# Performance work log

Hardware: AMD Instinct MI355X
Metric: run time of the kernel (lower is better)

Reference implementation:

```python
import jax, jax.numpy as jnp
import numpy as np

N_NODES = 100000
N_EDGES = 1600000
IN_DIM = 128
HID = 64
OUT_DIM = 3


def _glorot(key, shape):
    fan_in, fan_out = shape[0], shape[1]
    std = (2.0 / (fan_in + fan_out)) ** 0.5
    return jax.random.normal(key, shape, jnp.float32) * std


def setup_inputs() -> dict:
    key = jax.random.key(0)
    ks = jax.random.split(key, 12)
    x = jax.random.normal(ks[0], (N_NODES, IN_DIM), jnp.float32)
    edge_index = jax.random.randint(ks[1], (2, N_EDGES), 0, N_NODES, dtype=jnp.int32)
    return {
        "x": x,
        "edge_index": edge_index,
        "W1": _glorot(ks[2], (IN_DIM, HID)), "b1": jnp.zeros((HID,), jnp.float32),
        "W2": _glorot(ks[3], (HID, HID)), "b2": jnp.zeros((HID,), jnp.float32),
        "W3": _glorot(ks[4], (HID, HID)), "b3": jnp.zeros((HID,), jnp.float32),
        "W4": _glorot(ks[5], (HID, HID // 2)), "b4": jnp.zeros((HID // 2,), jnp.float32),
        "Wh": _glorot(ks[6], (HID // 2, OUT_DIM)), "bh": jnp.zeros((OUT_DIM,), jnp.float32),
    }


def reference(x, edge_index, W1, b1, W2, b2, W3, b3, W4, b4, Wh, bh):
    n = x.shape[0]
    self_loops = jnp.arange(n, dtype=edge_index.dtype)
    src = jnp.concatenate([edge_index[0], self_loops])  # message sources j
    dst = jnp.concatenate([edge_index[1], self_loops])  # aggregation targets i
    # symmetric GCN normalization with self-loops: deg over targets (unit edge weights)
    deg = jax.ops.segment_sum(jnp.ones_like(dst, jnp.float32), dst, num_segments=n)
    dinv = jnp.where(deg > 0, jax.lax.rsqrt(deg), 0.0)
    norm = dinv[src] * dinv[dst]  # [E+N]

    def gcn(h, W, b):
        h = h @ W  # transform first (PyG GCNConv order)
        agg = jax.ops.segment_sum(h[src] * norm[:, None], dst, num_segments=n)
        return agg + b

    h = jax.nn.relu(gcn(x, W1, b1))   # dropout is identity in eval mode
    h = jax.nn.relu(gcn(h, W2, b2))
    h = jax.nn.relu(gcn(h, W3, b3))
    h = jax.nn.relu(gcn(h, W4, b4))
    return h @ Wh + bh  # [N, 3]
```

## Files before the change

kernel.cpp:

```cpp
#include <hip/hip_runtime.h>
#include <hip/hip_bf16.h>
#include <hip/hip_fp16.h>
#include <cstdint>


#define MAXD 512
#define EB   8192
#define PADSLACK 2048

typedef _Float16 half8v __attribute__((ext_vector_type(8)));
typedef _Float16 half2v __attribute__((ext_vector_type(2)));
typedef float    float4v __attribute__((ext_vector_type(4)));

#if defined(__has_builtin)
#if __has_builtin(__builtin_amdgcn_fdot2)
#define HAVE_FDOT2 1
#endif
#endif

__device__ __forceinline__ float fdot2f(half2v a, half2v b, float c) {
#ifdef HAVE_FDOT2
    return __builtin_amdgcn_fdot2(a, b, c, false);
#else
    return c + (float)a[0] * (float)b[0] + (float)a[1] * (float)b[1];
#endif
}

__device__ __forceinline__ void digit_base_scan(const int* __restrict__ totals,
                                                int ND, int* pairs, int* cbs) {
    const int t = threadIdx.x;
    const int e0 = 2 * t, e1 = 2 * t + 1;
    int v0 = (e0 < ND) ? totals[e0] : 0;
    int v1 = (e1 < ND) ? totals[e1] : 0;
    pairs[t] = v0 + v1;
    __syncthreads();
    for (int off = 1; off < 256; off <<= 1) {
        int x = (t >= off) ? pairs[t - off] : 0;
        __syncthreads();
        pairs[t] += x;
        __syncthreads();
    }
    int ep = pairs[t] - v0 - v1;
    cbs[e0] = ep;
    cbs[e1] = ep + v0;
    __syncthreads();
}

__device__ __forceinline__ void hist_body(const int* __restrict__ ei,
                                          int* __restrict__ histM, int E, int b) {
    __shared__ int hist[MAXD];
    const int tid = threadIdx.x;
    hist[tid] = 0; hist[tid + 256] = 0;
    __syncthreads();
    const int base = b * EB;
#pragma unroll 2
    for (int it = 0; it < EB / 256; it += 4) {
        int d[4]; bool ok[4];
#pragma unroll
        for (int u = 0; u < 4; ++u) {
            int e = base + (it + u) * 256 + tid;
            ok[u] = e < E;
            d[u] = ok[u] ? ei[E + e] : 0;
        }
#pragma unroll
        for (int u = 0; u < 4; ++u)
            if (ok[u]) atomicAdd(&hist[d[u] >> 8], 1);
    }
    __syncthreads();
    histM[(size_t)b * MAXD + tid] = hist[tid];
    histM[(size_t)b * MAXD + tid + 256] = hist[tid + 256];
}

__global__ __launch_bounds__(256) void scan_digits_k(int* __restrict__ histM,
                                                     int* __restrict__ totals,
                                                     int NBLK) {
    __shared__ int s[256];
    const int t = threadIdx.x, dg = blockIdx.x;
    int v = (t < NBLK) ? histM[(size_t)t * MAXD + dg] : 0;
    s[t] = v;
    __syncthreads();
    for (int off = 1; off < 256; off <<= 1) {
        int x = (t >= off) ? s[t - off] : 0;
        __syncthreads();
        s[t] += x;
        __syncthreads();
    }
    if (t < NBLK) histM[(size_t)t * MAXD + dg] = s[t] - v;
    if (t == 255) totals[dg] = s[255];
}

template <int K, int OUT>
__device__ __forceinline__ void gemm_body(const float* __restrict__ H,
                                          const float* __restrict__ W,
                                          float* __restrict__ Tout, int n, int bx) {
    constexpr int TX  = OUT / 4;
    constexpr int TY  = 256 / TX;
    constexpr int BM  = TY * 4;
    constexpr int BK  = 32;
    constexpr int PAD = 4;

    __shared__ float At[BK][BM + PAD];
    __shared__ float Ws[BK][OUT];

    const int t    = threadIdx.x;
    const int cx   = t % TX;
    const int ry   = t / TX;
    const int row0 = bx * BM;

    float acc[4][4] = {{0.f}};
    const int arow = t >> 3;
    const int af4  = t & 7;

    for (int k0 = 0; k0 < K; k0 += BK) {
#pragma unroll
        for (int p = 0; p < BM / 32; ++p) {
            int r  = arow + p * 32;
            int gr = row0 + r;
            int grc = gr < n ? gr : n - 1;
            float4 v = *reinterpret_cast<const float4*>(
                H + (size_t)grc * K + k0 + af4 * 4);
            At[af4 * 4 + 0][r] = v.x;
            At[af4 * 4 + 1][r] = v.y;
            At[af4 * 4 + 2][r] = v.z;
            At[af4 * 4 + 3][r] = v.w;
        }
#pragma unroll
        for (int p = 0; p < (BK * OUT) / 1024; ++p) {
            int idx = t + p * 256;
            int wk  = idx / (OUT / 4);
            int wf  = idx % (OUT / 4);
            float4 v = *reinterpret_cast<const float4*>(
                W + (size_t)(k0 + wk) * OUT + wf * 4);
            *reinterpret_cast<float4*>(&Ws[wk][wf * 4]) = v;
        }
        __syncthreads();
#pragma unroll
        for (int k = 0; k < BK; ++k) {
            float4 a = *reinterpret_cast<const float4*>(&At[k][ry * 4]);
            float4 w = *reinterpret_cast<const float4*>(&Ws[k][cx * 4]);
            acc[0][0] = fmaf(a.x, w.x, acc[0][0]);
            acc[0][1] = fmaf(a.x, w.y, acc[0][1]);
            acc[0][2] = fmaf(a.x, w.z, acc[0][2]);
            acc[0][3] = fmaf(a.x, w.w, acc[0][3]);
            acc[1][0] = fmaf(a.y, w.x, acc[1][0]);
            acc[1][1] = fmaf(a.y, w.y, acc[1][1]);
            acc[1][2] = fmaf(a.y, w.z, acc[1][2]);
            acc[1][3] = fmaf(a.y, w.w, acc[1][3]);
            acc[2][0] = fmaf(a.z, w.x, acc[2][0]);
            acc[2][1] = fmaf(a.z, w.y, acc[2][1]);
            acc[2][2] = fmaf(a.z, w.z, acc[2][2]);
            acc[2][3] = fmaf(a.z, w.w, acc[2][3]);
            acc[3][0] = fmaf(a.w, w.x, acc[3][0]);
            acc[3][1] = fmaf(a.w, w.y, acc[3][1]);
            acc[3][2] = fmaf(a.w, w.z, acc[3][2]);
            acc[3][3] = fmaf(a.w, w.w, acc[3][3]);
        }
        __syncthreads();
    }
#pragma unroll
    for (int i = 0; i < 4; ++i) {
        int gr = row0 + ry * 4 + i;
        if (gr < n) {
            float4 v = make_float4(acc[i][0], acc[i][1], acc[i][2], acc[i][3]);
            *reinterpret_cast<float4*>(Tout + (size_t)gr * OUT + cx * 4) = v;
        }
    }
}

__device__ __forceinline__ void pack_body(const int* __restrict__ ei,
                                          const int* __restrict__ histM,
                                          const int* __restrict__ totals,
                                          int* __restrict__ packed,
                                          int E, int ND, int b) {
    __shared__ int pairs[256];
    __shared__ int cbs[MAXD];
    __shared__ int cur[MAXD];
    const int tid = threadIdx.x;
    digit_base_scan(totals, ND, pairs, cbs);
    for (int t = tid; t < ND; t += 256)
        cur[t] = cbs[t] + histM[(size_t)b * MAXD + t];
    __syncthreads();
    const int base = b * EB;
    for (int it = 0; it < EB / 256; it += 4) {
        int s[4], d[4]; bool ok[4];
#pragma unroll
        for (int u = 0; u < 4; ++u) {
            int e = base + (it + u) * 256 + tid;
            ok[u] = e < E;
            if (ok[u]) { s[u] = ei[e]; d[u] = ei[E + e]; }
        }
#pragma unroll
        for (int u = 0; u < 4; ++u) {
            if (ok[u]) {
                int pos = atomicAdd(&cur[d[u] >> 8], 1);
                packed[pos] = (s[u] << 8) | (d[u] & 255);
            }
        }
    }
}

__global__ __launch_bounds__(256) void hist_gemm1_k(
    const int* __restrict__ ei, int* __restrict__ histM, int E,
    const float* __restrict__ x, const float* __restrict__ W1,
    float* __restrict__ T1, int n, int NH) {
    const int bx = blockIdx.x;
    if (bx < NH) hist_body(ei, histM, E, bx);
    else         gemm_body<128, 64>(x, W1, T1, n, bx - NH);
}

__global__ __launch_bounds__(256) void pack_gemm1_k(
    const int* __restrict__ ei, const int* __restrict__ histM,
    const int* __restrict__ totals, int* __restrict__ packed,
    const float* __restrict__ x, const float* __restrict__ W1,
    float* __restrict__ T1, int n, int E, int ND, int NPB, int G1) {
    const int bx = blockIdx.x;
    if (bx < NPB) pack_body(ei, histM, totals, packed, E, ND, bx);
    else          gemm_body<128, 64>(x, W1, T1, n, G1 + bx - NPB);
}

__global__ __launch_bounds__(256) void bucket_k(const int* __restrict__ packed,
                                                const int* __restrict__ totals,
                                                int ND,
                                                int* __restrict__ col,
                                                int4* __restrict__ rpc,
                                                float* __restrict__ dinv,
                                                const float* __restrict__ Traw,
                                                __half* __restrict__ Th, int n) {
    __shared__ int   pairs[256];
    __shared__ int   cbs[MAXD];
    __shared__ int   hist[256];
    __shared__ int   pref[256];
    __shared__ int   cur[256];
    __shared__ float dinv_l[256];

    const int tid = threadIdx.x;
    const int dg  = blockIdx.x;
    digit_base_scan(totals, ND, pairs, cbs);
    const int base  = cbs[dg];
    const int m     = totals[dg];
    const int basep = base + dg * PADSLACK;

    hist[tid] = 0;
    __syncthreads();
    for (int k0 = 0; k0 < m; k0 += 1024) {
        int v[4]; bool ok[4];
#pragma unroll
        for (int u = 0; u < 4; ++u) {
            int k = k0 + u * 256 + tid;
            ok[u] = k < m;
            v[u] = ok[u] ? packed[base + k] : 0;
        }
#pragma unroll
        for (int u = 0; u < 4; ++u)
            if (ok[u]) atomicAdd(&hist[v[u] & 255], 1);
    }
    __syncthreads();
    const int deg   = hist[tid];
    const int cnt_p = (deg + 8) & ~7;
    pref[tid] = cnt_p;
    __syncthreads();
    for (int off = 1; off < 256; off <<= 1) {
        int x = (tid >= off) ? pref[tid - off] : 0;
        __syncthreads();
        pref[tid] += x;
        __syncthreads();
    }
    const int rp = basep + pref[tid] - cnt_p;
    const float di = rsqrtf((float)(deg + 1));
    dinv_l[tid] = di;
    cur[tid] = rp + 1;
    const int d = dg * 256 + tid;
    if (d < n) {
        rpc[d]  = make_int4(rp, cnt_p, __float_as_int(di), 0);
        dinv[d] = di;
        col[rp] = d;
        for (int k = deg + 1; k < cnt_p; ++k) col[rp + k] = n;
    }
    __syncthreads();
    for (int k0 = 0; k0 < m; k0 += 1024) {
        int v[4]; bool ok[4];
#pragma unroll
        for (int u = 0; u < 4; ++u) {
            int k = k0 + u * 256 + tid;
            ok[u] = k < m;
            v[u] = ok[u] ? packed[base + k] : 0;
        }
#pragma unroll
        for (int u = 0; u < 4; ++u) {
            if (ok[u]) {
                int pos = atomicAdd(&cur[v[u] & 255], 1);
                col[pos] = v[u] >> 8;
            }
        }
    }
    const int r0 = dg * 256;
#pragma unroll 4
    for (int it = 0; it < 16; ++it) {
        int idx = it * 256 + tid;
        int rl  = idx >> 4;
        int r   = r0 + rl;
        if (r < n) {
            float4 v = reinterpret_cast<const float4*>(Traw)[(size_t)r * 16 + (idx & 15)];
            float dd = dinv_l[rl];
            union { ushort4 u; __half h[4]; } pk;
            pk.h[0] = __float2half_rn(v.x * dd);
            pk.h[1] = __float2half_rn(v.y * dd);
            pk.h[2] = __float2half_rn(v.z * dd);
            pk.h[3] = __float2half_rn(v.w * dd);
            reinterpret_cast<ushort4*>(Th)[(size_t)r * 16 + (idx & 15)] = pk.u;
        }
    }
    if (dg == 0 && tid < 16) {
        uint2 z; z.x = 0u; z.y = 0u;
        reinterpret_cast<uint2*>(Th)[(size_t)n * 16 + tid] = z;
    }
}

template <int OUT>
__global__ __launch_bounds__(256) void gemm_mfma_k(
    const _Float16* __restrict__ H, const float* __restrict__ W,
    const float* __restrict__ dinv, _Float16* __restrict__ T, int n) {
    constexpr int NT = OUT / 16;
    const int lane = threadIdx.x & 63;
    const int m16  = lane & 15;
    const int quad = lane >> 4;
    const int wid  = (blockIdx.x * blockDim.x + threadIdx.x) >> 6;
    const int nw   = (gridDim.x * blockDim.x) >> 6;

    half8v bfrag[NT][2];
#pragma unroll
    for (int t = 0; t < NT; ++t)
#pragma unroll
        for (int h = 0; h < 2; ++h)
#pragma unroll
            for (int j = 0; j < 8; ++j)
                bfrag[t][h][j] = (_Float16)W[(size_t)(h * 32 + quad * 8 + j) * OUT
                                             + t * 16 + m16];

    const int nblk = (n + 15) >> 4;
    for (int rb = wid; rb < nblk; rb += nw) {
        const int r0 = rb * 16;
        int ra = r0 + m16; if (ra >= n) ra = n - 1;
        const half8v* hrow = reinterpret_cast<const half8v*>(H + (size_t)ra * 64);
        half8v a0 = hrow[quad];
        half8v a1 = hrow[4 + quad];

        float4v dfr[NT];
#pragma unroll
        for (int t = 0; t < NT; ++t) {
            float4v z = {0.f, 0.f, 0.f, 0.f};
            z = __builtin_amdgcn_mfma_f32_16x16x32_f16(a0, bfrag[t][0], z, 0, 0, 0);
            z = __builtin_amdgcn_mfma_f32_16x16x32_f16(a1, bfrag[t][1], z, 0, 0, 0);
            dfr[t] = z;
        }
#pragma unroll
        for (int reg = 0; reg < 4; ++reg) {
            int row = r0 + quad * 4 + reg;
            if (row < n) {
                float di = dinv[row];
#pragma unroll
                for (int t = 0; t < NT; ++t)
                    T[(size_t)row * 64 + t * 16 + m16] =
                        (_Float16)(dfr[t][reg] * di);
            }
        }
    }
}

template <int NB, int LR>
__device__ __forceinline__ void gather_batch(int c_l, const uint2* __restrict__ T2,
                                             int q, int sw, float4& acc, int g0) {
    constexpr int NSW = 64 / LR;
    constexpr int GPE = 8 / NSW;
    constexpr int NV  = NB * GPE;
    const half2v s10 = {(_Float16)1.f, (_Float16)0.f};
    const half2v s01 = {(_Float16)0.f, (_Float16)1.f};
    uint2 v[NV];
#pragma unroll
    for (int g = 0; g < NB; ++g)
#pragma unroll
        for (int u = 0; u < GPE; ++u) {
            int cc = __shfl(c_l, (g0 + g) * 8 + u * NSW + sw, 64);
            v[g * GPE + u] = T2[(size_t)cc * 16 + q];
        }
#pragma unroll
    for (int k = 0; k < NV; ++k) {
        union { uint2 uu; half2v h[2]; } cv; cv.uu = v[k];
        acc.x = fdot2f(cv.h[0], s10, acc.x);
        acc.y = fdot2f(cv.h[0], s01, acc.y);
        acc.z = fdot2f(cv.h[1], s10, acc.z);
        acc.w = fdot2f(cv.h[1], s01, acc.w);
    }
}

__device__ __forceinline__ void gather_node(int cnt, int start, int c_a,
                                            const uint2* __restrict__ T2,
                                            const int* __restrict__ col,
                                            int lane, int q, int sw, float4& acc) {
    if (cnt <= 64) {
        switch (cnt >> 3) {
            case 1: gather_batch<1, 64 / ((64/16))>(c_a, T2, q, sw, acc, 0); break;
            default: break;
        }
    }
}

template <int LR, bool FUSE_HEAD>
__global__ __launch_bounds__(256, 8) void agg_k(const __half* __restrict__ T,
                                             const int4* __restrict__ rpc,
                                             const int* __restrict__ col,
                                             const float* __restrict__ bias,
                                             void* __restrict__ O, int n,
                                             const float* __restrict__ Wh,
                                             const float* __restrict__ bh) {
    constexpr int NSW = 64 / LR;
    constexpr int GPE = 8 / NSW;
    const int lane = threadIdx.x & 63;
    const int q    = lane % LR;
    const int sw   = lane / LR;
    const int wid  = (blockIdx.x * blockDim.x + threadIdx.x) >> 6;
    const int nw   = (gridDim.x * blockDim.x) >> 6;
    if (wid >= n) return;

    const uint2* __restrict__ T2 = reinterpret_cast<const uint2*>(T);
    const float4 b4 = reinterpret_cast<const float4*>(bias)[q];

    int ib = wid + nw; if (ib >= n) ib = n - 1;
    int4 rc_a = rpc[wid];
    int4 rc_b = rpc[ib];
    int  c_a  = col[rc_a.x + lane];

    for (int i = wid; i < n; i += nw) {
        int ic = i + 2 * nw; if (ic >= n) ic = n - 1;
        int4 rc_c = rpc[ic];
        int  c_nx = col[rc_b.x + lane];

        const int   cnt   = rc_a.y;
        const int   start = rc_a.x;
        const float di    = __int_as_float(rc_a.z);

        float4 acc = make_float4(0.f, 0.f, 0.f, 0.f);
        if (cnt <= 64) {
            switch (cnt >> 3) {
                case 1: gather_batch<1, LR>(c_a, T2, q, sw, acc, 0); break;
                case 2: gather_batch<2, LR>(c_a, T2, q, sw, acc, 0); break;
                case 3: gather_batch<3, LR>(c_a, T2, q, sw, acc, 0); break;
                case 4: gather_batch<4, LR>(c_a, T2, q, sw, acc, 0); break;
                case 5: gather_batch<4, LR>(c_a, T2, q, sw, acc, 0);
                        gather_batch<1, LR>(c_a, T2, q, sw, acc, 4); break;
                case 6: gather_batch<4, LR>(c_a, T2, q, sw, acc, 0);
                        gather_batch<2, LR>(c_a, T2, q, sw, acc, 4); break;
                case 7: gather_batch<4, LR>(c_a, T2, q, sw, acc, 0);
                        gather_batch<3, LR>(c_a, T2, q, sw, acc, 4); break;
                default: gather_batch<4, LR>(c_a, T2, q, sw, acc, 0);
                         gather_batch<4, LR>(c_a, T2, q, sw, acc, 4); break;
            }
        } else {
            for (int base = 0; base < cnt; base += 64) {
                int m = cnt - base; if (m > 64) m = 64;
                int c_l = col[start + base + lane];
                for (int jg = 0; jg < m; jg += 32) {
                    int nb2 = (m - jg) >> 3; if (nb2 > 4) nb2 = 4;
                    int g0 = jg >> 3;
                    switch (nb2) {
                        case 1: gather_batch<1, LR>(c_l, T2, q, sw, acc, g0); break;
                        case 2: gather_batch<2, LR>(c_l, T2, q, sw, acc, g0); break;
                        case 3: gather_batch<3, LR>(c_l, T2, q, sw, acc, g0); break;
                        default: gather_batch<4, LR>(c_l, T2, q, sw, acc, g0); break;
                    }
                }
            }
        }
#pragma unroll
        for (int off = LR; off < 64; off <<= 1) {
            acc.x += __shfl_xor(acc.x, off, 64);
            acc.y += __shfl_xor(acc.y, off, 64);
            acc.z += __shfl_xor(acc.z, off, 64);
            acc.w += __shfl_xor(acc.w, off, 64);
        }
        float4 h;
        h.x = fmaxf(fmaf(di, acc.x, b4.x), 0.f);
        h.y = fmaxf(fmaf(di, acc.y, b4.y), 0.f);
        h.z = fmaxf(fmaf(di, acc.z, b4.z), 0.f);
        h.w = fmaxf(fmaf(di, acc.w, b4.w), 0.f);
        if constexpr (!FUSE_HEAD) {
            if (sw == 0) {
                union { ushort4 u; __half hh[4]; } pk;
                pk.hh[0] = __float2half_rn(h.x);
                pk.hh[1] = __float2half_rn(h.y);
                pk.hh[2] = __float2half_rn(h.z);
                pk.hh[3] = __float2half_rn(h.w);
                ushort* base_p = (ushort*)O + (size_t)i * 64;
                *reinterpret_cast<ushort4*>(base_p + 4 * q) = pk.u;
            }
        } else {
            float* Of = (float*)O;
            float p0 = h.x * Wh[(4 * q + 0) * 3 + 0];
            float p1 = h.x * Wh[(4 * q + 0) * 3 + 1];
            float p2 = h.x * Wh[(4 * q + 0) * 3 + 2];
            p0 = fmaf(h.y, Wh[(4 * q + 1) * 3 + 0], p0);
            p1 = fmaf(h.y, Wh[(4 * q + 1) * 3 + 1], p1);
            p2 = fmaf(h.y, Wh[(4 * q + 1) * 3 + 2], p2);
            p0 = fmaf(h.z, Wh[(4 * q + 2) * 3 + 0], p0);
            p1 = fmaf(h.z, Wh[(4 * q + 2) * 3 + 1], p1);
            p2 = fmaf(h.z, Wh[(4 * q + 2) * 3 + 2], p2);
            p0 = fmaf(h.w, Wh[(4 * q + 3) * 3 + 0], p0);
            p1 = fmaf(h.w, Wh[(4 * q + 3) * 3 + 1], p1);
            p2 = fmaf(h.w, Wh[(4 * q + 3) * 3 + 2], p2);
#pragma unroll
            for (int off = 1; off < LR; off <<= 1) {
                p0 += __shfl_xor(p0, off, 64);
                p1 += __shfl_xor(p1, off, 64);
                p2 += __shfl_xor(p2, off, 64);
            }
            if (lane == 0) {
                Of[(size_t)i * 3 + 0] = p0 + bh[0];
                Of[(size_t)i * 3 + 1] = p1 + bh[1];
                Of[(size_t)i * 3 + 2] = p2 + bh[2];
            }
        }
        rc_a = rc_b; rc_b = rc_c; c_a = c_nx;
    }
}

extern "C" void kernel_launch(void* const* d_in, const int* in_sizes, int n_in,
                              void* d_out, int out_size, void* d_ws, size_t ws_size,
                              hipStream_t stream) {
    const float* x  = (const float*)d_in[0];
    const int*   ei = (const int*)d_in[1];
    const float* W1 = (const float*)d_in[2];
    const float* b1 = (const float*)d_in[3];
    const float* W2 = (const float*)d_in[4];
    const float* b2 = (const float*)d_in[5];
    const float* W3 = (const float*)d_in[6];
    const float* b3 = (const float*)d_in[7];
    const float* W4 = (const float*)d_in[8];
    const float* b4 = (const float*)d_in[9];
    const float* Wh = (const float*)d_in[10];
    const float* bh = (const float*)d_in[11];
    float* out = (float*)d_out;

    const int n = in_sizes[0] / 128;
    const int E = in_sizes[1] / 2;
    const int ND   = (n + 255) / 256;
    const int NBLK = (E + EB - 1) / EB;

    char* ws = (char*)d_ws;
    auto alloc = [&](size_t bytes) {
        char* p = ws;
        ws += (bytes + 255) & ~(size_t)255;
        return p;
    };
    int*    histM  = (int*)alloc((size_t)NBLK * MAXD * 4);
    int*    totals = (int*)alloc((size_t)MAXD * 4);
    int*    packed = (int*)alloc((size_t)E * 4);
    int*    col    = (int*)alloc(((size_t)E + (size_t)ND * PADSLACK + 256) * 4);
    int4*   rpc    = (int4*)alloc((size_t)n * 16);
    float*  dinv   = (float*)alloc((size_t)n * 4);
    float*  bufF   = (float*)alloc((size_t)n * 64 * 4);
    __half* bufH   = (__half*)alloc(((size_t)n + 1) * 64 * 2);
    __half* bufG   = (__half*)bufF;

    dim3 blk(256);
    const int G  = (n + 63) / 64;
    const int G1 = G / 3;
    const int G2 = G - G1;
    const int agg_blocks = 2048;
    const int mfma_blocks = 640;

    hist_gemm1_k<<<dim3(NBLK + G1), blk, 0, stream>>>(ei, histM, E, x, W1, bufF, n, NBLK);
    scan_digits_k<<<dim3(ND), blk, 0, stream>>>(histM, totals, NBLK);
    pack_gemm1_k<<<dim3(NBLK + G2), blk, 0, stream>>>(ei, histM, totals, packed,
                                                      x, W1, bufF, n, E, ND, NBLK, G1);
    bucket_k<<<dim3(ND), blk, 0, stream>>>(packed, totals, ND, col, rpc,
                                           dinv, bufF, bufH, n);
    agg_k<16, false><<<dim3(agg_blocks), blk, 0, stream>>>(
        bufH, rpc, col, b1, bufG, n, nullptr, nullptr);
    gemm_mfma_k<64><<<dim3(mfma_blocks), blk, 0, stream>>>(
        (const _Float16*)bufG, W2, dinv, (_Float16*)bufH, n);
    agg_k<16, false><<<dim3(agg_blocks), blk, 0, stream>>>(
        bufH, rpc, col, b2, bufG, n, nullptr, nullptr);
    gemm_mfma_k<64><<<dim3(mfma_blocks), blk, 0, stream>>>(
        (const _Float16*)bufG, W3, dinv, (_Float16*)bufH, n);
    agg_k<16, false><<<dim3(agg_blocks), blk, 0, stream>>>(
        bufH, rpc, col, b3, bufG, n, nullptr, nullptr);
    gemm_mfma_k<32><<<dim3(mfma_blocks), blk, 0, stream>>>(
        (const _Float16*)bufG, W4, dinv, (_Float16*)bufH, n);
    agg_k<8, true><<<dim3(agg_blocks), blk, 0, stream>>>(
        bufH, rpc, col, b4, out, n, Wh, bh);
}
```

Before: 334.5 us.

## Software-pipeline neighbor gathers across nodes with double-buffered registers

Restructures the aggregation kernel so the first four groups of neighbor feature loads for the next node are issued before the current node's accumulation, using two register buffers that swap roles in an unrolled-by-two loop. Row-pointer and column prefetch depth is extended by one node. Launch bounds drop from 8 to 4 waves per SIMD to allow the larger register footprint. This aims to hide gather latency but reduces occupancy and raises register pressure.

```diff
diff --git a/kernel.cpp b/kernel.cpp
--- a/kernel.cpp
+++ b/kernel.cpp
@@ -368,6 +368,37 @@
 }
 
 template <int NB, int LR>
+__device__ __forceinline__ void gather_issue(int c_l, const uint2* __restrict__ T2,
+                                             int q, int sw, uint2* __restrict__ v) {
+    constexpr int NSW = 64 / LR;
+    constexpr int GPE = 8 / NSW;
+#pragma unroll
+    for (int g = 0; g < NB; ++g)
+#pragma unroll
+        for (int u = 0; u < GPE; ++u) {
+            int cc = __shfl(c_l, g * 8 + u * NSW + sw, 64);
+            v[g * GPE + u] = T2[(size_t)cc * 16 + q];
+        }
+}
+
+template <int NG, int LR>
+__device__ __forceinline__ void gather_fdot(const uint2* __restrict__ v, float4& acc) {
+    constexpr int NSW = 64 / LR;
+    constexpr int GPE = 8 / NSW;
+    constexpr int NV  = NG * GPE;
+    const half2v s10 = {(_Float16)1.f, (_Float16)0.f};
+    const half2v s01 = {(_Float16)0.f, (_Float16)1.f};
+#pragma unroll
+    for (int k = 0; k < NV; ++k) {
+        union { uint2 uu; half2v h[2]; } cv; cv.uu = v[k];
+        acc.x = fdot2f(cv.h[0], s10, acc.x);
+        acc.y = fdot2f(cv.h[0], s01, acc.y);
+        acc.z = fdot2f(cv.h[1], s10, acc.z);
+        acc.w = fdot2f(cv.h[1], s01, acc.w);
+    }
+}
+
+template <int NB, int LR>
 __device__ __forceinline__ void gather_batch(int c_l, const uint2* __restrict__ T2,
                                              int q, int sw, float4& acc, int g0) {
     constexpr int NSW = 64 / LR;
@@ -393,70 +424,43 @@
     }
 }
 
-__device__ __forceinline__ void gather_node(int cnt, int start, int c_a,
-                                            const uint2* __restrict__ T2,
-                                            const int* __restrict__ col,
-                                            int lane, int q, int sw, float4& acc) {
-    if (cnt <= 64) {
-        switch (cnt >> 3) {
-            case 1: gather_batch<1, 64 / ((64/16))>(c_a, T2, q, sw, acc, 0); break;
-            default: break;
-        }
-    }
-}
-
 template <int LR, bool FUSE_HEAD>
-__global__ __launch_bounds__(256, 8) void agg_k(const __half* __restrict__ T,
-                                             const int4* __restrict__ rpc,
-                                             const int* __restrict__ col,
-                                             const float* __restrict__ bias,
-                                             void* __restrict__ O, int n,
-                                             const float* __restrict__ Wh,
-                                             const float* __restrict__ bh) {
-    constexpr int NSW = 64 / LR;
-    constexpr int GPE = 8 / NSW;
-    const int lane = threadIdx.x & 63;
-    const int q    = lane % LR;
-    const int sw   = lane / LR;
-    const int wid  = (blockIdx.x * blockDim.x + threadIdx.x) >> 6;
-    const int nw   = (gridDim.x * blockDim.x) >> 6;
-    if (wid >= n) return;
-
-    const uint2* __restrict__ T2 = reinterpret_cast<const uint2*>(T);
-    const float4 b4 = reinterpret_cast<const float4*>(bias)[q];
-
-    int ib = wid + nw; if (ib >= n) ib = n - 1;
-    int4 rc_a = rpc[wid];
-    int4 rc_b = rpc[ib];
-    int  c_a  = col[rc_a.x + lane];
-
-    for (int i = wid; i < n; i += nw) {
-        int ic = i + 2 * nw; if (ic >= n) ic = n - 1;
-        int4 rc_c = rpc[ic];
-        int  c_nx = col[rc_b.x + lane];
-
-        const int   cnt   = rc_a.y;
-        const int   start = rc_a.x;
-        const float di    = __int_as_float(rc_a.z);
-
-        float4 acc = make_float4(0.f, 0.f, 0.f, 0.f);
-        if (cnt <= 64) {
-            switch (cnt >> 3) {
-                case 1: gather_batch<1, LR>(c_a, T2, q, sw, acc, 0); break;
-                case 2: gather_batch<2, LR>(c_a, T2, q, sw, acc, 0); break;
-                case 3: gather_batch<3, LR>(c_a, T2, q, sw, acc, 0); break;
-                case 4: gather_batch<4, LR>(c_a, T2, q, sw, acc, 0); break;
-                case 5: gather_batch<4, LR>(c_a, T2, q, sw, acc, 0);
-                        gather_batch<1, LR>(c_a, T2, q, sw, acc, 4); break;
-                case 6: gather_batch<4, LR>(c_a, T2, q, sw, acc, 0);
-                        gather_batch<2, LR>(c_a, T2, q, sw, acc, 4); break;
-                case 7: gather_batch<4, LR>(c_a, T2, q, sw, acc, 0);
-                        gather_batch<3, LR>(c_a, T2, q, sw, acc, 4); break;
-                default: gather_batch<4, LR>(c_a, T2, q, sw, acc, 0);
-                         gather_batch<4, LR>(c_a, T2, q, sw, acc, 4); break;
-            }
-        } else {
-            for (int base = 0; base < cnt; base += 64) {
+__device__ __forceinline__ void agg_body(
+    int i, int n, int nw, int lane, int q, int sw,
+    const uint2* __restrict__ T2, const int* __restrict__ col,
+    const int4* __restrict__ rpc,
+    int4& rcP, int4& rcQ, int4& rcR, int& cP, int& cQ,
+    uint2* __restrict__ vP, uint2* __restrict__ vQ,
+    const float4& b4, void* __restrict__ O,
+    const float* __restrict__ Wh, const float* __restrict__ bh) {
+    int iS = i + 3 * nw; if (iS >= n) iS = n - 1;
+    int4 rcS = rpc[iS];
+    int cR = col[rcR.x + lane];
+    {
+        int ng = rcQ.y >> 3; if (ng > 4) ng = 4;
+        switch (ng) {
+            case 1: gather_issue<1, LR>(cQ, T2, q, sw, vQ); break;
+            case 2: gather_issue<2, LR>(cQ, T2, q, sw, vQ); break;
+            case 3: gather_issue<3, LR>(cQ, T2, q, sw, vQ); break;
+            default: gather_issue<4, LR>(cQ, T2, q, sw, vQ); break;
+        }
+    }
+    const int   cnt = rcP.y;
+    const float di  = __int_as_float(rcP.z);
+    float4 acc = make_float4(0.f, 0.f, 0.f, 0.f);
+    switch (cnt >> 3) {
+        case 1: gather_fdot<1, LR>(vP, acc); break;
+        case 2: gather_fdot<2, LR>(vP, acc); break;
+        case 3: gather_fdot<3, LR>(vP, acc); break;
+        case 4: gather_fdot<4, LR>(vP, acc); break;
+        case 5: gather_fdot<4, LR>(vP, acc); gather_batch<1, LR>(cP, T2, q, sw, acc, 4); break;
+        case 6: gather_fdot<4, LR>(vP, acc); gather_batch<2, LR>(cP, T2, q, sw, acc, 4); break;
+        case 7: gather_fdot<4, LR>(vP, acc); gather_batch<3, LR>(cP, T2, q, sw, acc, 4); break;
+        default: {
+            gather_fdot<4, LR>(vP, acc);
+            gather_batch<4, LR>(cP, T2, q, sw, acc, 4);
+            const int start = rcP.x;
+            for (int base = 64; base < cnt; base += 64) {
                 int m = cnt - base; if (m > 64) m = 64;
                 int c_l = col[start + base + lane];
                 for (int jg = 0; jg < m; jg += 32) {
@@ -470,56 +474,108 @@
                     }
                 }
             }
-        }
-#pragma unroll
-        for (int off = LR; off < 64; off <<= 1) {
-            acc.x += __shfl_xor(acc.x, off, 64);
-            acc.y += __shfl_xor(acc.y, off, 64);
-            acc.z += __shfl_xor(acc.z, off, 64);
-            acc.w += __shfl_xor(acc.w, off, 64);
-        }
-        float4 h;
-        h.x = fmaxf(fmaf(di, acc.x, b4.x), 0.f);
-        h.y = fmaxf(fmaf(di, acc.y, b4.y), 0.f);
-        h.z = fmaxf(fmaf(di, acc.z, b4.z), 0.f);
-        h.w = fmaxf(fmaf(di, acc.w, b4.w), 0.f);
-        if constexpr (!FUSE_HEAD) {
-            if (sw == 0) {
-                union { ushort4 u; __half hh[4]; } pk;
-                pk.hh[0] = __float2half_rn(h.x);
-                pk.hh[1] = __float2half_rn(h.y);
-                pk.hh[2] = __float2half_rn(h.z);
-                pk.hh[3] = __float2half_rn(h.w);
-                ushort* base_p = (ushort*)O + (size_t)i * 64;
-                *reinterpret_cast<ushort4*>(base_p + 4 * q) = pk.u;
-            }
-        } else {
-            float* Of = (float*)O;
-            float p0 = h.x * Wh[(4 * q + 0) * 3 + 0];
-            float p1 = h.x * Wh[(4 * q + 0) * 3 + 1];
-            float p2 = h.x * Wh[(4 * q + 0) * 3 + 2];
-            p0 = fmaf(h.y, Wh[(4 * q + 1) * 3 + 0], p0);
-            p1 = fmaf(h.y, Wh[(4 * q + 1) * 3 + 1], p1);
-            p2 = fmaf(h.y, Wh[(4 * q + 1) * 3 + 2], p2);
-            p0 = fmaf(h.z, Wh[(4 * q + 2) * 3 + 0], p0);
-            p1 = fmaf(h.z, Wh[(4 * q + 2) * 3 + 1], p1);
-            p2 = fmaf(h.z, Wh[(4 * q + 2) * 3 + 2], p2);
-            p0 = fmaf(h.w, Wh[(4 * q + 3) * 3 + 0], p0);
-            p1 = fmaf(h.w, Wh[(4 * q + 3) * 3 + 1], p1);
-            p2 = fmaf(h.w, Wh[(4 * q + 3) * 3 + 2], p2);
-#pragma unroll
-            for (int off = 1; off < LR; off <<= 1) {
-                p0 += __shfl_xor(p0, off, 64);
-                p1 += __shfl_xor(p1, off, 64);
-                p2 += __shfl_xor(p2, off, 64);
-            }
-            if (lane == 0) {
-                Of[(size_t)i * 3 + 0] = p0 + bh[0];
-                Of[(size_t)i * 3 + 1] = p1 + bh[1];
-                Of[(size_t)i * 3 + 2] = p2 + bh[2];
-            }
-        }
-        rc_a = rc_b; rc_b = rc_c; c_a = c_nx;
+            break;
+        }
+    }
+#pragma unroll
+    for (int off = LR; off < 64; off <<= 1) {
+        acc.x += __shfl_xor(acc.x, off, 64);
+        acc.y += __shfl_xor(acc.y, off, 64);
+        acc.z += __shfl_xor(acc.z, off, 64);
+        acc.w += __shfl_xor(acc.w, off, 64);
+    }
+    float4 h;
+    h.x = fmaxf(fmaf(di, acc.x, b4.x), 0.f);
+    h.y = fmaxf(fmaf(di, acc.y, b4.y), 0.f);
+    h.z = fmaxf(fmaf(di, acc.z, b4.z), 0.f);
+    h.w = fmaxf(fmaf(di, acc.w, b4.w), 0.f);
+    if constexpr (!FUSE_HEAD) {
+        if (sw == 0) {
+            union { ushort4 u; __half hh[4]; } pk;
+            pk.hh[0] = __float2half_rn(h.x);
+            pk.hh[1] = __float2half_rn(h.y);
+            pk.hh[2] = __float2half_rn(h.z);
+            pk.hh[3] = __float2half_rn(h.w);
+            ushort* base_p = (ushort*)O + (size_t)i * 64;
+            *reinterpret_cast<ushort4*>(base_p + 4 * q) = pk.u;
+        }
+    } else {
+        float* Of = (float*)O;
+        float p0 = h.x * Wh[(4 * q + 0) * 3 + 0];
+        float p1 = h.x * Wh[(4 * q + 0) * 3 + 1];
+        float p2 = h.x * Wh[(4 * q + 0) * 3 + 2];
+        p0 = fmaf(h.y, Wh[(4 * q + 1) * 3 + 0], p0);
+        p1 = fmaf(h.y, Wh[(4 * q + 1) * 3 + 1], p1);
+        p2 = fmaf(h.y, Wh[(4 * q + 1) * 3 + 2], p2);
+        p0 = fmaf(h.z, Wh[(4 * q + 2) * 3 + 0], p0);
+        p1 = fmaf(h.z, Wh[(4 * q + 2) * 3 + 1], p1);
+        p2 = fmaf(h.z, Wh[(4 * q + 2) * 3 + 2], p2);
+        p0 = fmaf(h.w, Wh[(4 * q + 3) * 3 + 0], p0);
+        p1 = fmaf(h.w, Wh[(4 * q + 3) * 3 + 1], p1);
+        p2 = fmaf(h.w, Wh[(4 * q + 3) * 3 + 2], p2);
+#pragma unroll
+        for (int off = 1; off < LR; off <<= 1) {
+            p0 += __shfl_xor(p0, off, 64);
+            p1 += __shfl_xor(p1, off, 64);
+            p2 += __shfl_xor(p2, off, 64);
+        }
+        if (lane == 0) {
+            Of[(size_t)i * 3 + 0] = p0 + bh[0];
+            Of[(size_t)i * 3 + 1] = p1 + bh[1];
+            Of[(size_t)i * 3 + 2] = p2 + bh[2];
+        }
+    }
+    rcP = rcQ; rcQ = rcR; rcR = rcS;
+    cP = cQ; cQ = cR;
+}
+
+template <int LR, bool FUSE_HEAD>
+__global__ __launch_bounds__(256, 4) void agg_k(const __half* __restrict__ T,
+                                             const int4* __restrict__ rpc,
+                                             const int* __restrict__ col,
+                                             const float* __restrict__ bias,
+                                             void* __restrict__ O, int n,
+                                             const float* __restrict__ Wh,
+                                             const float* __restrict__ bh) {
+    constexpr int NSW = 64 / LR;
+    constexpr int GPE = 8 / NSW;
+    constexpr int NV  = 4 * GPE;
+    const int lane = threadIdx.x & 63;
+    const int q    = lane % LR;
+    const int sw   = lane / LR;
+    const int wid  = (blockIdx.x * blockDim.x + threadIdx.x) >> 6;
+    const int nw   = (gridDim.x * blockDim.x) >> 6;
+    if (wid >= n) return;
+
+    const uint2* __restrict__ T2 = reinterpret_cast<const uint2*>(T);
+    const float4 b4 = reinterpret_cast<const float4*>(bias)[q];
+
+    int i1 = wid + nw;     if (i1 >= n) i1 = n - 1;
+    int i2 = wid + 2 * nw; if (i2 >= n) i2 = n - 1;
+    int4 rcP = rpc[wid];
+    int4 rcQ = rpc[i1];
+    int4 rcR = rpc[i2];
+    int  cP  = col[rcP.x + lane];
+    int  cQ  = col[rcQ.x + lane];
+
+    uint2 vA[NV], vB[NV];
+#pragma unroll
+    for (int k = 0; k < NV; ++k) { vA[k] = make_uint2(0u, 0u); vB[k] = make_uint2(0u, 0u); }
+    {
+        int ng = rcP.y >> 3; if (ng > 4) ng = 4;
+        switch (ng) {
+            case 1: gather_issue<1, LR>(cP, T2, q, sw, vA); break;
+            case 2: gather_issue<2, LR>(cP, T2, q, sw, vA); break;
+            case 3: gather_issue<3, LR>(cP, T2, q, sw, vA); break;
+            default: gather_issue<4, LR>(cP, T2, q, sw, vA); break;
+        }
+    }
+    for (int i = wid; i < n; i += 2 * nw) {
+        agg_body<LR, FUSE_HEAD>(i, n, nw, lane, q, sw, T2, col, rpc,
+                                rcP, rcQ, rcR, cP, cQ, vA, vB, b4, O, Wh, bh);
+        if (i + nw < n)
+            agg_body<LR, FUSE_HEAD>(i + nw, n, nw, lane, q, sw, T2, col, rpc,
+                                    rcP, rcQ, rcR, cP, cQ, vB, vA, b4, O, Wh, bh);
     }
 }
 
```

Result: slower. 348.3 us (+4.1%).
